# Performance work log

Measured on AMD Instinct MI355X. Metric: run time of the kernel, lower is better.

## Reference

```python
import jax, jax.numpy as jnp
import numpy as np

COST_CLASS, COST_BBOX, COST_GIOU = 1.0, 5.0, 2.0


def _box_area(b):
    return (b[..., 2] - b[..., 0]) * (b[..., 3] - b[..., 1])


def _generalized_box_iou(b1, b2):
    # b1: (B,Q,4), b2: (B,N,4), xyxy -> (B,Q,N)
    a1 = _box_area(b1)[:, :, None]
    a2 = _box_area(b2)[:, None, :]
    lt = jnp.maximum(b1[:, :, None, :2], b2[:, None, :, :2])
    rb = jnp.minimum(b1[:, :, None, 2:], b2[:, None, :, 2:])
    wh = jnp.clip(rb - lt, 0.0)
    inter = wh[..., 0] * wh[..., 1]
    union = a1 + a2 - inter
    iou = inter / union
    lt_c = jnp.minimum(b1[:, :, None, :2], b2[:, None, :, :2])
    rb_c = jnp.maximum(b1[:, :, None, 2:], b2[:, None, :, 2:])
    wh_c = jnp.clip(rb_c - lt_c, 0.0)
    area_c = wh_c[..., 0] * wh_c[..., 1]
    return iou - (area_c - union) / area_c


@jax.jit
def _cost_matrix(pred_logits, pred_boxes, tgt_labels, tgt_boxes):
    B, Q, _ = pred_logits.shape
    N = tgt_labels.shape[1]
    out_prob = jax.nn.softmax(pred_logits, axis=-1)  # (B,Q,C+1)
    idx = jnp.broadcast_to(tgt_labels[:, None, :], (B, Q, N))
    cost_class = -jnp.take_along_axis(out_prob, idx, axis=-1)          # (B,Q,N)
    cost_bbox = jnp.abs(pred_boxes[:, :, None, :] - tgt_boxes[:, None, :, :]).sum(-1)  # L1 cdist
    cost_giou = -_generalized_box_iou(pred_boxes, tgt_boxes)
    return COST_CLASS * cost_class + COST_BBOX * cost_bbox + COST_GIOU * cost_giou


def _lsa(cost):
    """Shortest-augmenting-path Hungarian (Jonker-Volgenant style).
    cost: (n, m) with n <= m. Returns col4row[i] = assigned column of row i.
    Matches scipy.optimize.linear_sum_assignment (minimization)."""
    n, m = cost.shape
    INF = np.inf
    u = np.zeros(n + 1)
    v = np.zeros(m + 1)
    p = np.zeros(m + 1, dtype=np.int64)   # p[j] = row (1-indexed) assigned to col j
    way = np.zeros(m + 1, dtype=np.int64)
    for i in range(1, n + 1):
        p[0] = i
        j0 = 0
        minv = np.full(m + 1, INF)
        used = np.zeros(m + 1, dtype=bool)
        while True:
            used[j0] = True
            i0 = p[j0]
            cur = cost[i0 - 1] - u[i0] - v[1:]
            free = ~used[1:]
            upd = free & (cur < minv[1:])
            minv[1:][upd] = cur[upd]
            way[1:][upd] = j0
            cand = np.where(free, minv[1:], INF)
            j1 = int(np.argmin(cand)) + 1
            delta = cand[j1 - 1]
            uj = np.nonzero(used)[0]
            u[p[uj]] += delta
            v[uj] -= delta
            minv[~used] -= delta
            j0 = j1
            if p[j0] == 0:
                break
        while j0 != 0:
            j1 = way[j0]
            p[j0] = p[j1]
            j0 = j1
    col4row = np.zeros(n, dtype=np.int64)
    for j in range(1, m + 1):
        if p[j] != 0:
            col4row[p[j] - 1] = j - 1
    return col4row


def setup_inputs() -> dict:
    key = jax.random.key(0)
    k1, k2, k3, k4, k5 = jax.random.split(key, 5)
    B, Q, N, C1 = 64, 600, 80, 92

    def make_boxes(kx, ky, shape):
        xy = jax.random.uniform(kx, shape + (2,)) * 0.6
        wh = jax.random.uniform(ky, shape + (2,)) * 0.35 + 0.02
        return jnp.concatenate([xy, xy + wh], axis=-1)  # valid xyxy

    pred_logits = jax.random.normal(k1, (B, Q, C1), dtype=jnp.float32)
    pred_boxes = make_boxes(k2, k3, (B, Q))
    tgt_labels = jax.random.randint(k4, (B, N), 0, 91)
    tgt_boxes = make_boxes(k5, jax.random.fold_in(k5, 1), (B, N))
    return {"pred_logits": pred_logits, "pred_boxes": pred_boxes,
            "tgt_labels": tgt_labels, "tgt_boxes": tgt_boxes}


def reference(pred_logits, pred_boxes, tgt_labels, tgt_boxes):
    # Batched cost-matrix build on device, then host Hungarian per sample
    # (mirrors the original's .cpu().numpy() + scipy linear_sum_assignment).
    C = np.asarray(_cost_matrix(pred_logits, pred_boxes, tgt_labels, tgt_boxes))  # (B,Q,N)
    B, Q, N = C.shape
    rows = np.empty((B, N), dtype=np.int64)
    cols = np.empty((B, N), dtype=np.int64)
    for b in range(B):
        q_of_t = _lsa(C[b].T)              # transpose: N <= Q; query index per target
        order = np.argsort(q_of_t, kind="stable")
        rows[b] = q_of_t[order]            # sorted query (row) indices
        cols[b] = order                    # matching target (col) indices
    return jnp.asarray(rows), jnp.asarray(cols)
```

## Files before the change

### kernel.cpp

```cpp
#include <hip/hip_runtime.h>
#include <math.h>

#define BB 64
#define QQ 600
#define NT 80
#define NC 92
#define SLOTS 10
#define NTILE 10
#define NTHR 256
#define NWAVE 4
#define MAXROUNDS 16
#define STALLCAP 3


template <int CTRL>
__device__ __forceinline__ int dppi(int x) {
    return __builtin_amdgcn_update_dpp(x, x, CTRL, 0xF, 0xF, false);
}

__device__ __forceinline__ unsigned wave_min_u32(unsigned x) {
    unsigned y;
    y = (unsigned)dppi<0x121>((int)x); x = x < y ? x : y;
    y = (unsigned)dppi<0x122>((int)x); x = x < y ? x : y;
    y = (unsigned)dppi<0x124>((int)x); x = x < y ? x : y;
    y = (unsigned)dppi<0x128>((int)x); x = x < y ? x : y;
    y = (unsigned)__builtin_amdgcn_ds_swizzle((int)x, 0x401F); x = x < y ? x : y;
    y = (unsigned)__shfl_xor((int)x, 32); x = x < y ? x : y;
    return x;
}

__device__ __forceinline__ unsigned long long wave_min_key64(
        unsigned long long key, int* winlane) {
    const unsigned hi = (unsigned)(key >> 32), lo = (unsigned)key;
    const unsigned mhi = wave_min_u32(hi);
    unsigned long long t = __ballot(hi == mhi);
    unsigned mlo;
    if (__popcll(t) > 1) {
        mlo = wave_min_u32((hi == mhi) ? lo : 0xFFFFFFFFu);
        t = __ballot(hi == mhi && lo == mlo);
    } else {
        mlo = (unsigned)__shfl((int)lo, __builtin_ctzll(t));
    }
    *winlane = __builtin_ctzll(t);
    return ((unsigned long long)mhi << 32) | mlo;
}

__device__ __forceinline__ unsigned long long wave_min_key64_val(
        unsigned long long key) {
    const unsigned hi = (unsigned)(key >> 32), lo = (unsigned)key;
    const unsigned mhi = wave_min_u32(hi);
    const unsigned long long t = __ballot(hi == mhi);
    unsigned mlo;
    if (__popcll(t) > 1) mlo = wave_min_u32((hi == mhi) ? lo : 0xFFFFFFFFu);
    else                 mlo = (unsigned)__shfl((int)lo, __builtin_ctzll(t));
    return ((unsigned long long)mhi << 32) | mlo;
}

__device__ __forceinline__ unsigned f32_key(float f) {
    unsigned b = __float_as_uint(f);
    return b ^ ((unsigned)((int)b >> 31) | 0x80000000u);
}
__device__ __forceinline__ float key_f32(unsigned k) {
    unsigned b = (k & 0x80000000u) ? (k ^ 0x80000000u) : ~k;
    return __uint_as_float(b);
}
__device__ __forceinline__ unsigned long long f64_key(double d) {
    unsigned long long b = (unsigned long long)__double_as_longlong(d);
    return b ^ ((unsigned long long)((long long)b >> 63) | 0x8000000000000000ULL);
}
__device__ __forceinline__ double key_f64(unsigned long long k) {
    unsigned long long b = (k & 0x8000000000000000ULL) ? (k ^ 0x8000000000000000ULL) : ~k;
    return __longlong_as_double((long long)b);
}

__global__ __launch_bounds__(256) void phasea_kernel(
    const float* __restrict__ logits,
    const float* __restrict__ pboxes,
    const int*   __restrict__ tlabels,
    const float* __restrict__ tboxes,
    float* __restrict__ cost,
    float* __restrict__ pm1,
    float* __restrict__ pm2,
    int*   __restrict__ pmj)
{
    __shared__ float tile[64 * 93];
    __shared__ float s_pm[4 * 64], s_ps[4 * 64];
    __shared__ float s_tb[NT * 4];
    __shared__ int   s_tl[NT];

    const int g   = blockIdx.x;
    const int b   = g / NTILE;
    const int tix = g % NTILE;
    const int tid = threadIdx.x;
    const int qq  = tid & 63;
    const int wv  = tid >> 6;

    const int q0 = tix * 64;
    const int nq = min(64, QQ - q0);
    const float* src = logits + ((size_t)b * QQ + q0) * NC;
    for (int idx = tid; idx < nq * NC; idx += 256) {
        const int r = idx / NC;
        tile[r * 93 + (idx - r * NC)] = src[idx];
    }
    for (int i = tid; i < NT * 4; i += 256) s_tb[i] = tboxes[b * NT * 4 + i];
    for (int i = tid; i < NT;     i += 256) s_tl[i] = tlabels[b * NT + i];
    __syncthreads();

    {
        const int c0 = wv * 23;
        const float* r = &tile[qq * 93];
        float pm = r[c0];
        #pragma unroll 11
        for (int c = 1; c < 23; ++c) pm = fmaxf(pm, r[c0 + c]);
        s_pm[wv * 64 + qq] = pm;
    }
    __syncthreads();
    {
        const int c0 = wv * 23;
        float* r = &tile[qq * 93];
        const float m = fmaxf(fmaxf(s_pm[qq], s_pm[64 + qq]),
                              fmaxf(s_pm[128 + qq], s_pm[192 + qq]));
        float sum = 0.f;
        #pragma unroll 11
        for (int c = 0; c < 23; ++c) {
            const float e = expf(r[c0 + c] - m);
            r[c0 + c] = e;
            sum += e;
        }
        s_ps[wv * 64 + qq] = sum;
    }
    __syncthreads();

    const bool valid = qq < nq;
    float px1 = 0.f, py1 = 0.f, px2 = 0.f, py2 = 0.f, pa = 0.f, inv_s = 1.f;
    if (valid) {
        const float* pb = pboxes + ((size_t)b * QQ + q0 + qq) * 4;
        px1 = pb[0]; py1 = pb[1]; px2 = pb[2]; py2 = pb[3];
        pa  = (px2 - px1) * (py2 - py1);
        const float s = (s_ps[qq] + s_ps[64 + qq]) + (s_ps[128 + qq] + s_ps[192 + qq]);
        inv_s = 1.f / s;
    }
    float* crow = cost + (size_t)b * NT * QQ + q0 + qq;

    for (int tt = 0; tt < 20; ++tt) {
        const int t = wv * 20 + tt;
        float costv = INFINITY;
        if (valid) {
            const int lbl = s_tl[t];
            const float cc = -(tile[qq * 93 + lbl] * inv_s);
            const float tx1 = s_tb[t*4+0], ty1 = s_tb[t*4+1];
            const float tx2 = s_tb[t*4+2], ty2 = s_tb[t*4+3];
            const float cb = fabsf(px1-tx1) + fabsf(py1-ty1)
                           + fabsf(px2-tx2) + fabsf(py2-ty2);
            const float ta = (tx2 - tx1) * (ty2 - ty1);
            const float iw = fmaxf(fminf(px2, tx2) - fmaxf(px1, tx1), 0.f);
            const float ih = fmaxf(fminf(py2, ty2) - fmaxf(py1, ty1), 0.f);
            const float inter = iw * ih;
            const float uni   = pa + ta - inter;
            const float iou   = inter / uni;
            const float cw = fmaxf(fmaxf(px2, tx2) - fminf(px1, tx1), 0.f);
            const float ch = fmaxf(fmaxf(py2, ty2) - fminf(py1, ty1), 0.f);
            const float ac = cw * ch;
            const float giou = iou - (ac - uni) / ac;
            costv = (1.0f * cc + 5.0f * cb) + 2.0f * (-giou);
            crow[(size_t)t * QQ] = costv;
        }
        const unsigned key  = f32_key(costv);
        const unsigned kmin = wave_min_u32(key);
        const unsigned long long tied = __ballot(key == kmin);
        const int winlane = __builtin_ctzll(tied);
        const unsigned cand = (qq == winlane) ? 0xFFFFFFFFu : key;
        const unsigned k2   = wave_min_u32(cand);
        if (qq == 0) {
            const size_t idx = ((size_t)b * NT + t) * NTILE + tix;
            pm1[idx] = key_f32(kmin); pm2[idx] = key_f32(k2);
            pmj[idx] = q0 + winlane;
        }
    }
}

__global__ __launch_bounds__(256) void solver_kernel(
    const float* __restrict__ cost,
    const float* __restrict__ pm1,
    const float* __restrict__ pm2,
    const int*   __restrict__ pmj,
    int* __restrict__ rows_out,
    int* __restrict__ cols_out)
{
    __shared__ double vA[QQ];
    __shared__ double u[NT];
    __shared__ double bidm1[NT], bidm2[NT];
    __shared__ int    bidj[NT], bidver[NT];
    __shared__ int    pA[QQ];
    __shared__ int    verA[QQ];
    __shared__ int    colrow[QQ];
    __shared__ int    assigned[NT];
    __shared__ int    plist[NT];
    __shared__ int    pcnt;
    __shared__ int    wayA[QQ];
    __shared__ int    c4r[NT];
    __shared__ int    djkA[NT];

    const int b   = blockIdx.x;
    const int tid = threadIdx.x;
    const int qq  = tid & 63;
    const int wv  = tid >> 6;
    const float* C = cost + (size_t)b * NT * QQ;

    for (int c = tid; c < QQ; c += NTHR) { pA[c] = -1; verA[c] = 0; vA[c] = 0.0; }
    if (tid < NT) { assigned[tid] = 0; bidver[tid] = 0; }
    __syncthreads();

    if (tid < NT) {
        const int t = tid;
        const float* p1 = pm1 + ((size_t)b * NT + t) * NTILE;
        const float* p2 = pm2 + ((size_t)b * NT + t) * NTILE;
        const int*   pj = pmj + ((size_t)b * NT + t) * NTILE;
        float m1 = INFINITY, m2 = INFINITY; int j1 = QQ;
        for (int k = 0; k < NTILE; ++k) {
            const float a1 = p1[k], a2 = p2[k];
            const int   aj = pj[k];
            if (a1 < m1) { m2 = fminf(m1, a2); m1 = a1; j1 = aj; }
            else         { m2 = fminf(m2, a1); }
        }
        bidm1[t] = (double)m1; bidm2[t] = (double)m2; bidj[t] = j1;
        u[t] = (double)m1;
    }
    __syncthreads();

    int prev_np = 0x7fffffff, stall = 0;
    for (int round = 0; round < MAXROUNDS; ++round) {
        for (int c = tid; c < QQ; c += NTHR) colrow[c] = 0x7fffffff;
        if (tid == 0) pcnt = 0;
        __syncthreads();
        if (tid < NT && !assigned[tid]) {
            const int j = bidj[tid];
            if (bidver[tid] == verA[j]) atomicMin(&colrow[j], tid);
        }
        __syncthreads();
        if (tid < NT && !assigned[tid]) {
            const int i = tid, j = bidj[i];
            if (bidver[i] == verA[j] && colrow[j] == i) {
                const double m1 = bidm1[i], m2 = bidm2[i];
                const int prev = pA[j];
                pA[j] = i;
                verA[j] = verA[j] + 1;
                vA[j] -= (m2 - m1);
                u[i] = m2;
                assigned[i] = 1;
                if (prev >= 0) assigned[prev] = 0;
            }
        }
        __syncthreads();
        if (tid < NT && !assigned[tid]) { const int k = atomicAdd(&pcnt, 1); plist[k] = tid; }
        __syncthreads();
        const int np = pcnt;
        if (np == 0) break;
        if (np >= prev_np) { if (++stall >= STALLCAP) break; }
        else               { stall = 0; }
        prev_np = np;
        for (int idx = wv; idx < np; idx += NWAVE) {
            const int i = plist[idx];
            const float* rp = C + (size_t)i * QQ;
            float rowv[SLOTS];
            #pragma unroll
            for (int k = 0; k < SLOTS; ++k) { const int c = qq + 64*k; rowv[k] = (c < QQ) ? rp[c] : 0.f; }
            double m1 = INFINITY, m2 = INFINITY; int j1 = QQ;
            #pragma unroll
            for (int k = 0; k < SLOTS; ++k) {
                const int c = qq + 64 * k;
                if (c < QQ) {
                    const double key = (double)rowv[k] - vA[c];
                    if (key < m1)      { m2 = m1; m1 = key; j1 = c; }
                    else if (key < m2) { m2 = key; }
                }
            }
            int winlane;
            const unsigned long long kminv = wave_min_key64(f64_key(m1), &winlane);
            const unsigned long long c2 = (qq == winlane) ? f64_key(m2) : f64_key(m1);
            const unsigned long long k2minv = wave_min_key64_val(c2);
            const int jwin = __shfl(j1, winlane);
            if (qq == 0) {
                bidm1[i] = key_f64(kminv); bidm2[i] = key_f64(k2minv); bidj[i] = jwin;
                bidver[i] = verA[jwin];
                u[i] = key_f64(kminv);
            }
        }
        __syncthreads();
    }

    if (wv != 0) return;
    const int lane = qq;

    int nd = 0;
    for (int i = 0; i < NT; ++i) {
        if (!assigned[i]) { if (lane == 0) djkA[nd] = i; ++nd; }
    }

    double v_[SLOTS], minv_[SLOTS];
    int p_[SLOTS];
    #pragma unroll
    for (int k = 0; k < SLOTS; ++k) {
        const int c = lane + 64 * k;
        v_[k] = (c < QQ) ? vA[c] : 0.0;
        p_[k] = (c < QQ) ? pA[c] : -1;
    }

    float rowv[SLOTS];
    for (int ii = 0; ii < nd; ++ii) {
        const int i = djkA[ii];
        #pragma unroll
        for (int k = 0; k < SLOTS; ++k) minv_[k] = INFINITY;
        unsigned usedm = 0;
        int j0 = -1;
        double ui0 = u[i];
        {
            const float* rp = C + (size_t)i * QQ;
            #pragma unroll
            for (int k = 0; k < SLOTS; ++k) { const int c = lane + 64*k; rowv[k] = (c < QQ) ? rp[c] : 0.f; }
        }
        int j1, i1;

        for (;;) {
            if (j0 >= 0 && (j0 & 63) == lane) usedm |= 1u << (j0 >> 6);

            double bestv = INFINITY; int bestc = QQ;
            #pragma unroll
            for (int k = 0; k < SLOTS; ++k) {
                const int c = lane + 64 * k;
                if (c < QQ && !((usedm >> k) & 1u)) {
                    const double cur = ((double)rowv[k] - ui0) - v_[k];
                    if (cur < minv_[k]) { minv_[k] = cur; wayA[c] = j0; }
                    if (minv_[k] < bestv) { bestv = minv_[k]; bestc = c; }
                }
            }
            int winlane;
            const unsigned long long kminv = wave_min_key64(f64_key(bestv), &winlane);
            const double delta = key_f64(kminv);
            j1 = __shfl(bestc, winlane);

            {
                const int slot = j1 >> 6, lj = j1 & 63;
                int myp = p_[0];
                #pragma unroll
                for (int k = 1; k < SLOTS; ++k) if (slot == k) myp = p_[k];
                i1 = __shfl(myp, lj);
            }

            double ui_next = 0.0;
            float rown[SLOTS];
            if (i1 >= 0) {
                ui_next = u[i1];
                const float* rp = C + (size_t)i1 * QQ;
                #pragma unroll
                for (int k = 0; k < SLOTS; ++k) { const int c = lane + 64*k; rown[k] = (c < QQ) ? rp[c] : 0.f; }
            }

            #pragma unroll
            for (int k = 0; k < SLOTS; ++k) {
                const int c = lane + 64 * k;
                if (c < QQ) {
                    if ((usedm >> k) & 1u) { v_[k] -= delta; u[p_[k]] += delta; }
                    else                     minv_[k] -= delta;
                }
            }
            if (lane == 0) u[i] += delta;

            j0 = j1;
            if (i1 < 0) break;
            ui0 = ui_next;
            #pragma unroll
            for (int k = 0; k < SLOTS; ++k) rowv[k] = rown[k];
        }

        if (lane == 0) {
            int jj = j1;
            while (jj >= 0) {
                const int pr = wayA[jj];
                pA[jj] = (pr < 0) ? i : pA[pr];
                jj = pr;
            }
        }
        #pragma unroll
        for (int k = 0; k < SLOTS; ++k) {
            const int c = lane + 64 * k;
            p_[k] = (c < QQ) ? pA[c] : -1;
        }
    }

    #pragma unroll
    for (int k = 0; k < SLOTS; ++k) {
        const int c = lane + 64 * k;
        if (c < QQ) { const int t = pA[c]; if (t >= 0) c4r[t] = c; }
    }
    for (int t = lane; t < NT; t += 64) {
        const int c = c4r[t];
        int rank = 0;
        for (int t2 = 0; t2 < NT; ++t2) rank += (c4r[t2] < c) ? 1 : 0;
        rows_out[b * NT + rank] = c;
        cols_out[b * NT + rank] = t;
    }
}

extern "C" void kernel_launch(void* const* d_in, const int* in_sizes, int n_in,
                              void* d_out, int out_size, void* d_ws, size_t ws_size,
                              hipStream_t stream) {
    (void)in_sizes; (void)n_in; (void)out_size; (void)ws_size;
    const float* logits  = (const float*)d_in[0];
    const float* pboxes  = (const float*)d_in[1];
    const int*   tlabels = (const int*)d_in[2];
    const float* tboxes  = (const float*)d_in[3];
    float* cost = (float*)d_ws;
    float* pm1  = cost + (size_t)BB * NT * QQ;
    float* pm2  = pm1  + (size_t)BB * NT * NTILE;
    int*   pmj  = (int*)(pm2 + (size_t)BB * NT * NTILE);
    int*   out  = (int*)d_out;

    phasea_kernel<<<dim3(BB * NTILE), NTHR, 0, stream>>>(
        logits, pboxes, tlabels, tboxes, cost, pm1, pm2, pmj);
    solver_kernel<<<dim3(BB), NTHR, 0, stream>>>(
        cost, pm1, pm2, pmj, out, out + BB * NT);
}
```

Before: 108.1 us.

## Defer Hungarian dual updates to the end of each augmenting-path search

Replaces the per-iteration dual and minv adjustments in the shortest-augmenting-path loop with a lazily accumulated base offset. The candidate reduced costs are shifted by the running minimum, and the v/u duals of scanned columns are corrected once after the path ends, using dfin - minv. This removes a per-step pass over all slots and its scattered writes to u[], at the cost of a slightly different floating-point accumulation order. That could change tie-breaking in rare near-equal cases. It also drops the explicit next-row prefetch buffer, so the next row is now loaded directly into rowv.

```diff
diff --git a/kernel.cpp b/kernel.cpp
--- a/kernel.cpp
+++ b/kernel.cpp
@@ -314,12 +314,14 @@
         unsigned usedm = 0;
         int j0 = -1;
         double ui0 = u[i];
+        double base = 0.0;
         {
             const float* rp = C + (size_t)i * QQ;
             #pragma unroll
             for (int k = 0; k < SLOTS; ++k) { const int c = lane + 64*k; rowv[k] = (c < QQ) ? rp[c] : 0.f; }
         }
-        int j1, i1;
+        int j1 = -1, i1;
+        double dfin = 0.0;
 
         for (;;) {
             if (j0 >= 0 && (j0 & 63) == lane) usedm |= 1u << (j0 >> 6);
@@ -329,14 +331,14 @@
             for (int k = 0; k < SLOTS; ++k) {
                 const int c = lane + 64 * k;
                 if (c < QQ && !((usedm >> k) & 1u)) {
-                    const double cur = ((double)rowv[k] - ui0) - v_[k];
-                    if (cur < minv_[k]) { minv_[k] = cur; wayA[c] = j0; }
+                    const double cand = base + (((double)rowv[k] - ui0) - v_[k]);
+                    if (cand < minv_[k]) { minv_[k] = cand; wayA[c] = j0; }
                     if (minv_[k] < bestv) { bestv = minv_[k]; bestc = c; }
                 }
             }
             int winlane;
             const unsigned long long kminv = wave_min_key64(f64_key(bestv), &winlane);
-            const double delta = key_f64(kminv);
+            const double dmin = key_f64(kminv);
             j1 = __shfl(bestc, winlane);
 
             {
@@ -347,31 +349,28 @@
                 i1 = __shfl(myp, lj);
             }
 
-            double ui_next = 0.0;
-            float rown[SLOTS];
-            if (i1 >= 0) {
-                ui_next = u[i1];
+            if (i1 < 0) { dfin = dmin; break; }
+
+            ui0 = u[i1];
+            base = dmin;
+            {
                 const float* rp = C + (size_t)i1 * QQ;
                 #pragma unroll
-                for (int k = 0; k < SLOTS; ++k) { const int c = lane + 64*k; rown[k] = (c < QQ) ? rp[c] : 0.f; }
-            }
-
-            #pragma unroll
-            for (int k = 0; k < SLOTS; ++k) {
-                const int c = lane + 64 * k;
-                if (c < QQ) {
-                    if ((usedm >> k) & 1u) { v_[k] -= delta; u[p_[k]] += delta; }
-                    else                     minv_[k] -= delta;
-                }
-            }
-            if (lane == 0) u[i] += delta;
-
+                for (int k = 0; k < SLOTS; ++k) { const int c = lane + 64*k; rowv[k] = (c < QQ) ? rp[c] : 0.f; }
+            }
             j0 = j1;
-            if (i1 < 0) break;
-            ui0 = ui_next;
-            #pragma unroll
-            for (int k = 0; k < SLOTS; ++k) rowv[k] = rown[k];
-        }
+        }
+
+        #pragma unroll
+        for (int k = 0; k < SLOTS; ++k) {
+            const int c = lane + 64 * k;
+            if (c < QQ && ((usedm >> k) & 1u)) {
+                const double adj = dfin - minv_[k];
+                v_[k] -= adj;
+                u[p_[k]] += adj;
+            }
+        }
+        if (lane == 0) u[i] += dfin;
 
         if (lane == 0) {
             int jj = j1;
```

Result: no change. 108.8 us (+0.7%).
